# Kernel optimization log

Hardware: AMD Instinct MI355X
Metric: run time of the kernel (lower is better)

The kernel has to match this reference:

```python
import math
import jax, jax.numpy as jnp
import numpy as np

B, T, C, NB = 2, 2048, 512, 4
EPS = 1.1920929e-7  # torch.finfo(float32).eps, used by F.rms_norm default


def rms_norm(x):
    return x * jax.lax.rsqrt(jnp.mean(x * x, axis=-1, keepdims=True) + EPS)


def rope(x):
    # standard rotary embedding over the last dim; x: (..., T, C)
    t_len, c = x.shape[-2], x.shape[-1]
    half = c // 2
    inv_freq = 1.0 / (10000.0 ** (jnp.arange(half, dtype=jnp.float32) / half))
    ang = jnp.arange(t_len, dtype=jnp.float32)[:, None] * inv_freq[None, :]  # (T, half)
    cos, sin = jnp.cos(ang), jnp.sin(ang)
    x1, x2 = x[..., :half], x[..., half:]
    return jnp.concatenate([x1 * cos - x2 * sin, x2 * cos + x1 * sin], axis=-1)


def setup_inputs() -> dict:
    key = jax.random.key(0)
    ks = jax.random.split(key, 8)
    sc = 1.0 / math.sqrt(C)
    return {
        "a": jax.random.normal(ks[0], (B, T, C), jnp.float32),
        "x": jax.random.normal(ks[1], (B, T, C), jnp.float32),
        "Wq": jax.random.normal(ks[2], (C, NB * C), jnp.float32) * sc,
        "Wk": jax.random.normal(ks[3], (C, C), jnp.float32) * sc,
        "Wv": jax.random.normal(ks[4], (C, NB * C), jnp.float32) * sc,
        "Wo": jax.random.normal(ks[5], (C, C), jnp.float32) * sc,
        "v_sink_residual": jax.random.normal(ks[6], (1, 1, 1, C), jnp.float32) * 0.02,
        "v_sink_basis": jax.random.normal(ks[7], (1, NB, 1, C), jnp.float32) * 0.02,
    }


def reference(a, x, Wq, Wk, Wv, Wo, v_sink_residual, v_sink_basis):
    # projections
    q = (a @ Wq).reshape(B, T, NB, C).transpose(0, 2, 1, 3)  # (B,NB,T,C)
    q = rms_norm(q)
    v = (a @ Wv).reshape(B, T, NB, C).transpose(0, 2, 1, 3)  # (B,NB,T,C)
    k = x @ Wk  # (B,T,C), single branch
    q, k = rope(q), rope(k)

    att = jnp.einsum('bntc,bsc->bnts', q, k) / math.sqrt(C)  # (B,NB,T,T)
    causal = jnp.tril(jnp.ones((T, T), dtype=bool))
    att = jnp.where(causal, att, -jnp.inf)

    # branch-axis softmax; fully-masked (non-causal) columns are all -inf -> nan -> 0
    m = jax.lax.stop_gradient(jnp.max(att, axis=1, keepdims=True))
    e = jnp.exp(att - m)
    soft_probs = jnp.nan_to_num(e / jnp.sum(e, axis=1, keepdims=True))

    # hard argmax routing with straight-through estimator
    max_val = jnp.max(soft_probs, axis=1, keepdims=True)
    hard_mask = (soft_probs == max_val).astype(soft_probs.dtype)
    route_mask = jax.lax.stop_gradient(hard_mask - soft_probs) + soft_probs  # (B,NB,T,T)

    # softplus gating on per-position max score
    scores_max = jnp.max(att, axis=1)          # (B,T,T)
    s = jax.nn.softplus(scores_max)            # softplus(-inf) = 0 on masked
    S = jnp.sum(s, axis=-1, keepdims=True)
    scale = jnp.minimum(1.0 / (S + 1e-6), 1.0)
    w = s * scale                              # (B,T,T)
    residual = 1.0 - jnp.sum(w, axis=-1, keepdims=True)  # (B,T,1)

    combined_weights = w[:, None] * route_mask           # (B,NB,T,T)
    y_context = jnp.einsum('bnts,bnsc->bntc', combined_weights, v)
    branch_activity = jnp.max(route_mask, axis=-1, keepdims=True)  # (B,NB,T,1)
    y_basis = branch_activity * v_sink_basis               # (B,NB,T,C)
    y_branches = jnp.sum(y_context + y_basis, axis=1)      # (B,T,C)
    y_res = residual * v_sink_residual[:, 0]               # (B,T,1)*(1,1,C) -> (B,T,C)
    y = y_branches + y_res
    return y @ Wo
```

## Files before the change

### kernel.cpp

```cpp
#include <hip/hip_runtime.h>
#include <math.h>

#define B_    2
#define T_    2048
#define C_    512
#define NB_   4
#define HALF_ 256
#define BT_   (B_*T_)
#define EPS_  1.1920929e-07f
#define RSC_  0.044194173824159216f

using f32x4 = __attribute__((ext_vector_type(4))) float;
using s16x8 = __attribute__((ext_vector_type(8))) short;
using u16x8 = __attribute__((ext_vector_type(8))) unsigned short;

__device__ __forceinline__ unsigned short f2bf(float f) {
    unsigned x = __float_as_uint(f);
    unsigned r = (x + 0x7fffu + ((x >> 16) & 1u)) >> 16;
    return (unsigned short)r;
}
__device__ __forceinline__ float bf2f(unsigned short h) {
    return __uint_as_float(((unsigned)h) << 16);
}

__device__ __forceinline__ void gl16(const void* g, void* l) {
    __builtin_amdgcn_global_load_lds(
        (const __attribute__((address_space(1))) unsigned int*)g,
        (__attribute__((address_space(3))) unsigned int*)l, 16, 0, 0);
}

template<int N> __device__ __forceinline__ void wait_vm() {
    if constexpr (N == 0)      asm volatile("s_waitcnt vmcnt(0)" ::: "memory");
    else if constexpr (N == 4) asm volatile("s_waitcnt vmcnt(4)" ::: "memory");
    else                       asm volatile("s_waitcnt vmcnt(8)" ::: "memory");
}
__device__ __forceinline__ void wait_lgkm0() {
    asm volatile("s_waitcnt lgkmcnt(0)" ::: "memory");
}
__device__ __forceinline__ void bar() { __builtin_amdgcn_s_barrier(); }
__device__ __forceinline__ void sbar0() { __builtin_amdgcn_sched_barrier(0); }

__global__ __launch_bounds__(256) void rope_table_k(float* __restrict__ cosT,
                                                    float* __restrict__ sinT) {
    int t = blockIdx.x;
    int i = threadIdx.x;
    float ex   = (float)i / (float)HALF_;
    float invf = 1.0f / powf(10000.0f, ex);
    float ang  = (float)t * invf;
    float sv, cv;
    sincosf(ang, &sv, &cv);
    cosT[t*HALF_ + i] = cv;
    sinT[t*HALF_ + i] = sv;
}

__global__ __launch_bounds__(256) void cast2_hilo_k(const float* __restrict__ a,
                                                    const float* __restrict__ x,
                                                    unsigned short* __restrict__ ahi,
                                                    unsigned short* __restrict__ alo,
                                                    unsigned short* __restrict__ xhi,
                                                    unsigned short* __restrict__ xlo) {
    int i = blockIdx.x * 256 + threadIdx.x;
    const float* src; unsigned short *hi, *lo;
    if (i < 524288) { src = a; hi = ahi; lo = alo; }
    else { i -= 524288; src = x; hi = xhi; lo = xlo; }
    float4 v = ((const float4*)src)[i];
    ushort4 h, l;
    h.x = f2bf(v.x); l.x = f2bf(v.x - bf2f(h.x));
    h.y = f2bf(v.y); l.y = f2bf(v.y - bf2f(h.y));
    h.z = f2bf(v.z); l.z = f2bf(v.z - bf2f(h.z));
    h.w = f2bf(v.w); l.w = f2bf(v.w - bf2f(h.w));
    ((ushort4*)hi)[i] = h;
    ((ushort4*)lo)[i] = l;
}

__global__ __launch_bounds__(256) void tcast_k(const float* __restrict__ W,
                                               unsigned short* __restrict__ Whi,
                                               unsigned short* __restrict__ Wlo,
                                               int K, int N, int wantLo) {
    __shared__ float tile[64][65];
    int nbt = N >> 6;
    int nb = blockIdx.x % nbt, kb = blockIdx.x / nbt;
    int tid = threadIdx.x;
    int ty = tid >> 6, tx = tid & 63;
    for (int i = ty; i < 64; i += 4)
        tile[i][tx] = W[(size_t)(kb*64 + i) * N + nb*64 + tx];
    __syncthreads();
    for (int j = ty; j < 64; j += 4) {
        float v = tile[tx][j];
        unsigned short h = f2bf(v);
        size_t o = (size_t)(nb*64 + j) * K + kb*64 + tx;
        Whi[o] = h;
        if (wantLo) Wlo[o] = f2bf(v - bf2f(h));
    }
}

template<int SPLIT>
__global__ __launch_bounds__(256, SPLIT ? 2 : 4) void mm_k(
    const unsigned short* __restrict__ Ahi, const unsigned short* __restrict__ Alo,
    const unsigned short* __restrict__ Bhi, const unsigned short* __restrict__ Blo,
    float* __restrict__ C, int M, int N, int K)
{
    constexpr int BUFS = SPLIT ? 16384 : 8192;
    __shared__ __align__(16) short smem[2 * BUFS];

    int tid = threadIdx.x;
    int w = tid >> 6, l = tid & 63;
    int wm = w >> 1, wn = w & 1;
    int llo = l & 15, lhi = l >> 4;
    int rl8 = l >> 3, sl8 = l & 7;
    int nwg = gridDim.x;
    int bid = blockIdx.x;
    int sb = (bid & 7) * (nwg >> 3) + (bid >> 3);
    int nbt = N >> 7;
    int bx = sb % nbt, by = sb / nbt;
    int m0 = by << 7, n0 = bx << 7;

    const unsigned short* hs[4];
    const unsigned short* ls[4];
    int dst_[4];
    #pragma unroll
    for (int c = 0; c < 4; c++) {
        int r = (w << 5) + (c << 3) + rl8;
        int sp = sl8 ^ (r & 7);
        size_t off = (sp < 4) ? ((size_t)(m0 + r) * K + (sp << 3))
                              : ((size_t)(n0 + r) * K + ((sp - 4) << 3));
        hs[c] = (sp < 4 ? Ahi : Bhi) + off;
        if constexpr (SPLIT) ls[c] = (sp < 4 ? Alo : Blo) + off;
        dst_[c] = (w << 11) + (c << 9);
    }
    auto STAGE = [&](int cur, int k0) {
        short* base = smem + cur * BUFS;
        #pragma unroll
        for (int c = 0; c < 4; c++) {
            gl16(hs[c] + k0, base + dst_[c]);
            if constexpr (SPLIT) gl16(ls[c] + k0, base + 8192 + dst_[c]);
        }
    };

    f32x4 acc[4][4];
    #pragma unroll
    for (int mi = 0; mi < 4; mi++)
        #pragma unroll
        for (int ni = 0; ni < 4; ni++) acc[mi][ni] = (f32x4){0.f,0.f,0.f,0.f};

    const int NK = K >> 5;
    STAGE(0, 0);
    int cur = 0;
    for (int k = 0; k < NK; k++) {
        if (k + 1 < NK) { STAGE(cur ^ 1, (k + 1) << 5); wait_vm<SPLIT ? 8 : 4>(); }
        else wait_vm<0>();
        bar(); sbar0();
        short* Mh = smem + cur * BUFS;
        short* Ml = Mh + 8192;
        s16x8 bh[4], bl[4];
        #pragma unroll
        for (int ni = 0; ni < 4; ni++) {
            int br = (wn << 6) + (ni << 4) + llo;
            int bo = (br << 6) + (((lhi | 4) ^ (br & 7)) << 3);
            bh[ni] = *(const s16x8*)&Mh[bo];
            if constexpr (SPLIT) bl[ni] = *(const s16x8*)&Ml[bo];
        }
        #pragma unroll
        for (int mi = 0; mi < 4; mi++) {
            int ar = (wm << 6) + (mi << 4) + llo;
            int ao = (ar << 6) + ((lhi ^ (ar & 7)) << 3);
            s16x8 ah = *(const s16x8*)&Mh[ao];
            s16x8 al;
            if constexpr (SPLIT) al = *(const s16x8*)&Ml[ao];
            #pragma unroll
            for (int ni = 0; ni < 4; ni++) {
                acc[mi][ni] = __builtin_amdgcn_mfma_f32_16x16x32_bf16(ah, bh[ni], acc[mi][ni], 0, 0, 0);
                if constexpr (SPLIT) {
                    acc[mi][ni] = __builtin_amdgcn_mfma_f32_16x16x32_bf16(ah, bl[ni], acc[mi][ni], 0, 0, 0);
                    acc[mi][ni] = __builtin_amdgcn_mfma_f32_16x16x32_bf16(al, bh[ni], acc[mi][ni], 0, 0, 0);
                }
            }
        }
        wait_lgkm0(); sbar0(); bar();
        cur ^= 1;
    }
    #pragma unroll
    for (int mi = 0; mi < 4; mi++) {
        int row0 = m0 + (wm << 6) + (mi << 4) + (lhi << 2);
        #pragma unroll
        for (int ni = 0; ni < 4; ni++) {
            int col = n0 + (wn << 6) + (ni << 4) + llo;
            f32x4 v = acc[mi][ni];
            #pragma unroll
            for (int r = 0; r < 4; r++)
                C[(size_t)(row0 + r) * N + col] = v[r];
        }
    }
}

__global__ __launch_bounds__(256, 4) void mm_v_k(
    const unsigned short* __restrict__ Ahi,
    const unsigned short* __restrict__ Bhi,
    unsigned short* __restrict__ Vt, int M, int N, int K)
{
    __shared__ __align__(16) short smem[2 * 8192];
    int tid = threadIdx.x;
    int w = tid >> 6, l = tid & 63;
    int wm = w >> 1, wn = w & 1;
    int llo = l & 15, lhi = l >> 4;
    int rl8 = l >> 3, sl8 = l & 7;
    int nwg = gridDim.x;
    int bid = blockIdx.x;
    int sb = (bid & 7) * (nwg >> 3) + (bid >> 3);
    int nbt = N >> 7;
    int bx = sb % nbt, by = sb / nbt;
    int m0 = by << 7, n0 = bx << 7;

    const unsigned short* hs[4];
    int dst_[4];
    #pragma unroll
    for (int c = 0; c < 4; c++) {
        int r = (w << 5) + (c << 3) + rl8;
        int sp = sl8 ^ (r & 7);
        size_t off = (sp < 4) ? ((size_t)(m0 + r) * K + (sp << 3))
                              : ((size_t)(n0 + r) * K + ((sp - 4) << 3));
        hs[c] = (sp < 4 ? Ahi : Bhi) + off;
        dst_[c] = (w << 11) + (c << 9);
    }
    auto STAGE = [&](int cur, int k0) {
        short* base = smem + cur * 8192;
        #pragma unroll
        for (int c = 0; c < 4; c++) gl16(hs[c] + k0, base + dst_[c]);
    };

    f32x4 acc[4][4];
    #pragma unroll
    for (int mi = 0; mi < 4; mi++)
        #pragma unroll
        for (int ni = 0; ni < 4; ni++) acc[mi][ni] = (f32x4){0.f,0.f,0.f,0.f};

    const int NK = K >> 5;
    STAGE(0, 0);
    int cur = 0;
    for (int k = 0; k < NK; k++) {
        if (k + 1 < NK) { STAGE(cur ^ 1, (k + 1) << 5); wait_vm<4>(); }
        else wait_vm<0>();
        bar(); sbar0();
        short* Mh = smem + cur * 8192;
        s16x8 bh[4];
        #pragma unroll
        for (int ni = 0; ni < 4; ni++) {
            int br = (wn << 6) + (ni << 4) + llo;
            bh[ni] = *(const s16x8*)&Mh[(br << 6) + (((lhi | 4) ^ (br & 7)) << 3)];
        }
        #pragma unroll
        for (int mi = 0; mi < 4; mi++) {
            int ar = (wm << 6) + (mi << 4) + llo;
            s16x8 ah = *(const s16x8*)&Mh[(ar << 6) + ((lhi ^ (ar & 7)) << 3)];
            #pragma unroll
            for (int ni = 0; ni < 4; ni++)
                acc[mi][ni] = __builtin_amdgcn_mfma_f32_16x16x32_bf16(ah, bh[ni], acc[mi][ni], 0, 0, 0);
        }
        wait_lgkm0(); sbar0(); bar();
        cur ^= 1;
    }
    #pragma unroll
    for (int mi = 0; mi < 4; mi++) {
        int row0 = m0 + (wm << 6) + (mi << 4) + (lhi << 2);
        int b = row0 >> 11, t = row0 & (T_ - 1);
        #pragma unroll
        for (int ni = 0; ni < 4; ni++) {
            int col = n0 + (wn << 6) + (ni << 4) + llo;
            f32x4 v = acc[mi][ni];
            ushort4 o;
            o.x = f2bf(v[0]); o.y = f2bf(v[1]); o.z = f2bf(v[2]); o.w = f2bf(v[3]);
            *(ushort4*)(Vt + ((size_t)(b*(NB_*C_) + col)) * T_ + t) = o;
        }
    }
}

__global__ __launch_bounds__(256) void q_post3_k(const float* __restrict__ Qf,
                                                 const float* __restrict__ cosT,
                                                 const float* __restrict__ sinT,
                                                 unsigned short* __restrict__ Qhi,
                                                 unsigned short* __restrict__ Qlo) {
    int bt = blockIdx.x;
    int t  = bt & (T_ - 1);
    int w = threadIdx.x >> 6, l = threadIdx.x & 63;
    const float* row = Qf + (size_t)bt * (NB_*C_) + (w << 9);
    int i0 = l << 2;
    float4 x1 = *(const float4*)(row + i0);
    float4 x2 = *(const float4*)(row + i0 + HALF_);
    float s = x1.x*x1.x + x1.y*x1.y + x1.z*x1.z + x1.w*x1.w
            + x2.x*x2.x + x2.y*x2.y + x2.z*x2.z + x2.w*x2.w;
    #pragma unroll
    for (int mask = 1; mask <= 32; mask <<= 1) s += __shfl_xor(s, mask, 64);
    float r = rsqrtf(s * (1.0f / (float)C_) + EPS_);
    float4 cv = *(const float4*)(cosT + t*HALF_ + i0);
    float4 sv = *(const float4*)(sinT + t*HALF_ + i0);
    float v1[4], v2[4];
    v1[0] = x1.x*r*cv.x - x2.x*r*sv.x;  v2[0] = x2.x*r*cv.x + x1.x*r*sv.x;
    v1[1] = x1.y*r*cv.y - x2.y*r*sv.y;  v2[1] = x2.y*r*cv.y + x1.y*r*sv.y;
    v1[2] = x1.z*r*cv.z - x2.z*r*sv.z;  v2[2] = x2.z*r*cv.z + x1.z*r*sv.z;
    v1[3] = x1.w*r*cv.w - x2.w*r*sv.w;  v2[3] = x2.w*r*cv.w + x1.w*r*sv.w;
    size_t o = (size_t)bt * (NB_*C_) + (w << 9) + i0;
    ushort4 h1, h2, l1, l2;
    h1.x = f2bf(v1[0]); l1.x = f2bf(v1[0] - bf2f(h1.x));
    h1.y = f2bf(v1[1]); l1.y = f2bf(v1[1] - bf2f(h1.y));
    h1.z = f2bf(v1[2]); l1.z = f2bf(v1[2] - bf2f(h1.z));
    h1.w = f2bf(v1[3]); l1.w = f2bf(v1[3] - bf2f(h1.w));
    h2.x = f2bf(v2[0]); l2.x = f2bf(v2[0] - bf2f(h2.x));
    h2.y = f2bf(v2[1]); l2.y = f2bf(v2[1] - bf2f(h2.y));
    h2.z = f2bf(v2[2]); l2.z = f2bf(v2[2] - bf2f(h2.z));
    h2.w = f2bf(v2[3]); l2.w = f2bf(v2[3] - bf2f(h2.w));
    *(ushort4*)(Qhi + o)          = h1;
    *(ushort4*)(Qhi + o + HALF_)  = h2;
    *(ushort4*)(Qlo + o)          = l1;
    *(ushort4*)(Qlo + o + HALF_)  = l2;
}

__global__ __launch_bounds__(256) void k_post3_k(const float* __restrict__ Kf,
                                                 const float* __restrict__ cosT,
                                                 const float* __restrict__ sinT,
                                                 unsigned short* __restrict__ Khi,
                                                 unsigned short* __restrict__ Klo) {
    int sub = threadIdx.x >> 7, l = threadIdx.x & 127;
    int bt = blockIdx.x * 2 + sub;
    int t  = bt & (T_ - 1);
    const float* row = Kf + (size_t)bt * C_;
    int i0 = l << 1;
    float2 x1 = *(const float2*)(row + i0);
    float2 x2 = *(const float2*)(row + i0 + HALF_);
    float2 cv = *(const float2*)(cosT + t*HALF_ + i0);
    float2 sv = *(const float2*)(sinT + t*HALF_ + i0);
    float v1x = x1.x*cv.x - x2.x*sv.x, v2x = x2.x*cv.x + x1.x*sv.x;
    float v1y = x1.y*cv.y - x2.y*sv.y, v2y = x2.y*cv.y + x1.y*sv.y;
    size_t o = (size_t)bt * C_ + i0;
    ushort2 h1, h2, l1, l2;
    h1.x = f2bf(v1x); l1.x = f2bf(v1x - bf2f(h1.x));
    h1.y = f2bf(v1y); l1.y = f2bf(v1y - bf2f(h1.y));
    h2.x = f2bf(v2x); l2.x = f2bf(v2x - bf2f(h2.x));
    h2.y = f2bf(v2y); l2.y = f2bf(v2y - bf2f(h2.y));
    *(ushort2*)(Khi + o)         = h1;
    *(ushort2*)(Khi + o + HALF_) = h2;
    *(ushort2*)(Klo + o)         = l1;
    *(ushort2*)(Klo + o + HALF_) = l2;
}

__global__ __launch_bounds__(256, 2) void qk_routing_k(
    const unsigned short* __restrict__ Qhi, const unsigned short* __restrict__ Qlo,
    const unsigned short* __restrict__ Khi, const unsigned short* __restrict__ Klo,
    unsigned short* __restrict__ P, float* __restrict__ partS, unsigned* __restrict__ partA)
{
    __shared__ __align__(16) short smem[32768];

    int tid = threadIdx.x;
    int w = tid >> 6, l = tid & 63;
    int wm = w >> 1, wn = w & 1;
    int llo = l & 15, lhi = l >> 4;
    int rl8 = l >> 3, sl8 = l & 7;

    int bid = blockIdx.x;
    int j = (bid & 7) * 136 + (bid >> 3);
    int b = (j >= 544) ? 1 : 0;
    int j2 = j - 544 * b;
    int q = (int)((sqrtf(1.0f + 2.0f*(float)j2) - 1.0f) * 0.5f);
    if (2*(q+1)*(q+2) <= j2) q++;
    if (2*q*(q+1) > j2) q--;
    int r0 = j2 - 2*q*(q+1);
    int tloc = r0 / (q+1);
    int st = r0 - tloc*(q+1);
    int tt = (q << 2) + tloc;
    int t0 = tt << 5, s0 = st << 7;

    const unsigned short* hsrc[4];
    const unsigned short* lsrc[4];
    int dst_[4];
    #pragma unroll
    for (int c = 0; c < 4; c++) {
        int r = (w << 5) + (c << 3) + rl8;
        int sp = sl8 ^ (r & 7);
        size_t off = (sp < 4)
            ? ((size_t)(b*T_ + t0 + (r >> 2)) * (NB_*C_) + ((r & 3) << 9) + (sp << 3))
            : ((size_t)(b*T_ + s0 + r) * C_ + ((sp - 4) << 3));
        hsrc[c] = (sp < 4 ? Qhi : Khi) + off;
        lsrc[c] = (sp < 4 ? Qlo : Klo) + off;
        dst_[c] = (w << 11) + (c << 9);
    }
    auto STAGE = [&](int cur, int k0) {
        short* base = smem + (cur << 14);
        #pragma unroll
        for (int c = 0; c < 4; c++) {
            gl16(hsrc[c] + k0, base + dst_[c]);
            gl16(lsrc[c] + k0, base + 8192 + dst_[c]);
        }
    };

    f32x4 acc[4][4];
    #pragma unroll
    for (int mi = 0; mi < 4; mi++)
        #pragma unroll
        for (int ni = 0; ni < 4; ni++) acc[mi][ni] = (f32x4){0.f,0.f,0.f,0.f};

    STAGE(0, 0);
    int cur = 0;
    for (int k = 0; k < 16; k++) {
        if (k + 1 < 16) { STAGE(cur ^ 1, (k + 1) << 5); wait_vm<8>(); }
        else wait_vm<0>();
        bar(); sbar0();
        short* Mh = smem + (cur << 14);
        short* Ml = Mh + 8192;
        s16x8 bh[4], bl[4];
        #pragma unroll
        for (int ni = 0; ni < 4; ni++) {
            int br = (wn << 6) + (ni << 4) + llo;
            int bo = (br << 6) + (((lhi | 4) ^ (br & 7)) << 3);
            bh[ni] = *(const s16x8*)&Mh[bo];
            bl[ni] = *(const s16x8*)&Ml[bo];
        }
        #pragma unroll
        for (int mi = 0; mi < 4; mi++) {
            int ar = (wm << 6) + (mi << 4) + llo;
            int ao = (ar << 6) + ((lhi ^ (ar & 7)) << 3);
            s16x8 ah = *(const s16x8*)&Mh[ao];
            s16x8 al = *(const s16x8*)&Ml[ao];
            #pragma unroll
            for (int ni = 0; ni < 4; ni++) {
                acc[mi][ni] = __builtin_amdgcn_mfma_f32_16x16x32_bf16(ah, bh[ni], acc[mi][ni], 0, 0, 0);
                acc[mi][ni] = __builtin_amdgcn_mfma_f32_16x16x32_bf16(ah, bl[ni], acc[mi][ni], 0, 0, 0);
                acc[mi][ni] = __builtin_amdgcn_mfma_f32_16x16x32_bf16(al, bh[ni], acc[mi][ni], 0, 0, 0);
            }
        }
        wait_lgkm0(); sbar0(); bar();
        cur ^= 1;
    }
    __syncthreads();

    short* Pl = smem;
    #pragma unroll
    for (int mi = 0; mi < 4; mi++) {
        int tl = (wm << 4) + (mi << 2) + lhi;
        int tg = t0 + tl;
        float wsum = 0.f; unsigned ab = 0u;
        #pragma unroll
        for (int ni = 0; ni < 4; ni++) {
            int sl = (wn << 6) + (ni << 4) + llo;
            int sg = s0 + sl;
            f32x4 v = acc[mi][ni];
            float wu = 0.f; unsigned bits = 0u;
            if (sg <= tg) {
                float a0 = v[0]*RSC_, a1 = v[1]*RSC_, a2 = v[2]*RSC_, a3 = v[3]*RSC_;
                float m = fmaxf(fmaxf(a0, a1), fmaxf(a2, a3));
                bits = (a0 == m ? 1u : 0u) | (a1 == m ? 2u : 0u)
                     | (a2 == m ? 4u : 0u) | (a3 == m ? 8u : 0u);
                wu = fmaxf(m, 0.f) + log1pf(expf(-fabsf(m)));
                wsum += wu; ab |= bits;
            }
            unsigned short wub = f2bf(wu);
            Pl[(0*32 + tl)*136 + sl] = (bits & 1u) ? (short)wub : (short)0;
            Pl[(1*32 + tl)*136 + sl] = (bits & 2u) ? (short)wub : (short)0;
            Pl[(2*32 + tl)*136 + sl] = (bits & 4u) ? (short)wub : (short)0;
            Pl[(3*32 + tl)*136 + sl] = (bits & 8u) ? (short)wub : (short)0;
        }
        #pragma unroll
        for (int mask = 1; mask <= 8; mask <<= 1) wsum += __shfl_xor(wsum, mask, 64);
        int ai = (int)ab;
        #pragma unroll
        for (int mask = 1; mask <= 8; mask <<= 1) ai |= __shfl_xor(ai, mask, 64);
        if (llo == 0) {
            size_t pidx = ((((size_t)(b*64 + tt) * 16 + st) * 2 + wn) * 32) + tl;
            partS[pidx] = wsum;
            partA[pidx] = (unsigned)ai;
        }
    }
    __syncthreads();
    for (int i = tid; i < 2048; i += 256) {
        int row = i >> 4, g8 = i & 15;
        int n = row >> 5, tl = row & 31;
        u16x8 v = *(const u16x8*)&Pl[row*136 + (g8 << 3)];
        *(u16x8*)(P + ((size_t)((b*4 + n)*T_ + t0 + tl)) * T_ + s0 + (g8 << 3)) = v;
    }
}

__global__ __launch_bounds__(256, 2) void pv_k(
    const unsigned short* __restrict__ P, const unsigned short* __restrict__ Vt,
    unsigned short* __restrict__ py)
{
    __shared__ __align__(16) short smem[32768];
    int tid = threadIdx.x;
    int w = tid >> 6, l = tid & 63;
    int wm = w >> 1, wn = w & 1;
    int llo = l & 15, lhi = l >> 4;
    int rl = l >> 3, gs8 = l & 7;
    int rb = w << 5;
    int bid = blockIdx.x;
    int ph = bid & 3, cc = (bid >> 2) & 3, tt = 15 - ((bid >> 4) & 15), b = bid >> 8;
    int t0 = tt << 7, c0 = cc << 7;
    int b4 = b * 4;
    size_t bV = (size_t)b * (NB_*C_);

    size_t pa_[4], pb_[4];
    int dsb_[4];
    #pragma unroll
    for (int i8 = 0; i8 < 4; i8++) {
        int r = rb + (i8 << 3) + rl;
        int sg = (gs8 ^ (r & 7)) << 3;
        pa_[i8] = (size_t)(t0 + r) * T_ + sg;
        pb_[i8] = (size_t)(c0 + r) * T_ + sg;
        dsb_[i8] = (rb + (i8 << 3)) << 6;
    }
    auto STAGE = [&](int cur, int n, int k0) {
        short* base = smem + (cur << 14);
        size_t na = (size_t)(b4 + n) * T_ * T_;
        size_t nb = (bV + (size_t)(n << 9)) * T_;
        #pragma unroll
        for (int i8 = 0; i8 < 4; i8++) {
            gl16(P  + na + pa_[i8] + k0, base + dsb_[i8]);
            gl16(Vt + nb + pb_[i8] + k0, base + 8192 + dsb_[i8]);
        }
    };

    f32x4 acc[4][4];
    #pragma unroll
    for (int mi = 0; mi < 4; mi++)
        #pragma unroll
        for (int ni = 0; ni < 4; ni++) acc[mi][ni] = (f32x4){0.f,0.f,0.f,0.f};

    int first_sb = ph << 7;
    int num_sb = (first_sb <= t0 + 127) ? (((t0 + 127 - first_sb) >> 9) + 1) : 0;
    int nsteps = num_sb << 3;

    if (nsteps > 0) {
        int n_p = 0, sb_p = first_sb, h_p = 0;
        auto ADV = [&]() {
            h_p ^= 1;
            if (!h_p) { sb_p += 512; if (sb_p > t0 + 127) { sb_p = first_sb; n_p++; } }
        };
        STAGE(0, n_p, sb_p + (h_p << 6)); ADV();
        int cur = 0;
        for (int s = 0; s < nsteps; s++) {
            if (s + 1 < nsteps) { STAGE(cur ^ 1, n_p, sb_p + (h_p << 6)); ADV(); wait_vm<8>(); }
            else wait_vm<0>();
            bar(); sbar0();
            short* Ah = smem + (cur << 14);
            short* Bh = Ah + 8192;
            #pragma unroll
            for (int ks = 0; ks < 2; ks++) {
                s16x8 bh[4];
                #pragma unroll
                for (int ni = 0; ni < 4; ni++) {
                    int br = (wn << 6) + (ni << 4) + llo;
                    bh[ni] = *(const s16x8*)&Bh[br*64 + ((((ks << 2) + lhi) ^ (br & 7)) << 3)];
                }
                #pragma unroll
                for (int mi = 0; mi < 4; mi++) {
                    int ar = (wm << 6) + (mi << 4) + llo;
                    s16x8 ah = *(const s16x8*)&Ah[ar*64 + ((((ks << 2) + lhi) ^ (ar & 7)) << 3)];
                    #pragma unroll
                    for (int ni = 0; ni < 4; ni++)
                        acc[mi][ni] = __builtin_amdgcn_mfma_f32_16x16x32_bf16(ah, bh[ni], acc[mi][ni], 0, 0, 0);
                }
            }
            wait_lgkm0(); sbar0(); bar();
            cur ^= 1;
        }
    }
    unsigned short* out = py + (size_t)ph * (BT_*(size_t)C_);
    #pragma unroll
    for (int mi = 0; mi < 4; mi++) {
        int row0 = t0 + (wm << 6) + (mi << 4) + (lhi << 2);
        #pragma unroll
        for (int ni = 0; ni < 4; ni++) {
            int col = c0 + (wn << 6) + (ni << 4) + llo;
            f32x4 v = acc[mi][ni];
            #pragma unroll
            for (int r = 0; r < 4; r++)
                out[(size_t)(b*T_ + row0 + r) * C_ + col] = f2bf(v[r]);
        }
    }
}

__global__ __launch_bounds__(256) void combine3_k(
    const unsigned short* __restrict__ py, const float* __restrict__ partS,
    const unsigned* __restrict__ partA,
    const float* __restrict__ basis, const float* __restrict__ resid_sink,
    unsigned short* __restrict__ ybf)
{
    int bt = blockIdx.x;
    int t = bt & (T_ - 1);
    int b = bt >> 11;
    int i = threadIdx.x;
    int tt32 = t >> 5, tl = t & 31;
    int stmax = tt32 >> 2;
    float S = 0.f; unsigned act = 0u;
    for (int st = 0; st <= stmax; st++) {
        #pragma unroll
        for (int wn = 0; wn < 2; wn++) {
            size_t idx = ((((size_t)(b*64 + tt32) * 16 + st) * 2 + wn) * 32) + tl;
            S += partS[idx];
            act |= partA[idx];
        }
    }
    float y0 = 0.f, y1 = 0.f;
    #pragma unroll
    for (int ph = 0; ph < 4; ph++) {
        y0 += bf2f(py[(size_t)ph * (BT_*(size_t)C_) + (size_t)bt * C_ + i]);
        y1 += bf2f(py[(size_t)ph * (BT_*(size_t)C_) + (size_t)bt * C_ + i + 256]);
    }
    float scale = fminf(1.0f / (S + 1e-6f), 1.0f);
    float residual = 1.0f - scale * S;
    if (t < T_ - 1) act = 0xFu;
    float o0 = scale * y0, o1 = scale * y1;
    #pragma unroll
    for (int n = 0; n < 4; n++) if ((act >> n) & 1u) {
        o0 += basis[n*C_ + i];
        o1 += basis[n*C_ + i + 256];
    }
    o0 += residual * resid_sink[i];
    o1 += residual * resid_sink[i + 256];
    ybf[(size_t)bt * C_ + i]       = f2bf(o0);
    ybf[(size_t)bt * C_ + i + 256] = f2bf(o1);
}

extern "C" void kernel_launch(void* const* d_in, const int* in_sizes, int n_in,
                              void* d_out, int out_size, void* d_ws, size_t ws_size,
                              hipStream_t stream) {
    const float* a    = (const float*)d_in[0];
    const float* x    = (const float*)d_in[1];
    const float* Wq   = (const float*)d_in[2];
    const float* Wk   = (const float*)d_in[3];
    const float* Wv   = (const float*)d_in[4];
    const float* Wo   = (const float*)d_in[5];
    const float* vres = (const float*)d_in[6];
    const float* vbas = (const float*)d_in[7];

    float* ws = (float*)d_ws;
    float* cosT = ws;
    float* sinT = cosT + 524288;
    float* Qf   = sinT + 524288;
    float* Kf   = Qf + 8388608;
    unsigned short* ahi  = (unsigned short*)(Kf + 2097152);
    unsigned short* alo  = ahi  + 2097152;
    unsigned short* xhi  = alo  + 2097152;
    unsigned short* xlo  = xhi  + 2097152;
    unsigned short* Wqth = xlo  + 2097152;
    unsigned short* Wqtl = Wqth + 1048576;
    unsigned short* Wkth = Wqtl + 1048576;
    unsigned short* Wktl = Wkth + 262144;
    unsigned short* Wvth = Wktl + 262144;
    unsigned short* Woth = Wvth + 1048576;
    unsigned short* Qhi  = Woth + 262144;
    unsigned short* Qlo  = Qhi  + 8388608;
    unsigned short* Khi  = Qlo  + 8388608;
    unsigned short* Klo  = Khi  + 2097152;
    unsigned short* Vt   = Klo  + 2097152;
    unsigned short* P    = Vt   + 8388608;

    unsigned short* py = (unsigned short*)Qf;
    float* partS = Kf;
    unsigned* partA = (unsigned*)(Kf + 131072);
    unsigned short* ybf = (unsigned short*)(Kf + 262144);

    rope_table_k<<<T_, 256, 0, stream>>>(cosT, sinT);
    cast2_hilo_k<<<4096, 256, 0, stream>>>(a, x, ahi, alo, xhi, xlo);
    tcast_k<<<256, 256, 0, stream>>>(Wq, Wqth, Wqtl, 512, 2048, 1);
    tcast_k<<<64,  256, 0, stream>>>(Wk, Wkth, Wktl, 512, 512,  1);
    tcast_k<<<256, 256, 0, stream>>>(Wv, Wvth, nullptr, 512, 2048, 0);
    tcast_k<<<64,  256, 0, stream>>>(Wo, Woth, nullptr, 512, 512,  0);

    mm_k<1><<<512, 256, 0, stream>>>(ahi, alo, Wqth, Wqtl, Qf, BT_, 2048, 512);
    mm_k<1><<<128, 256, 0, stream>>>(xhi, xlo, Wkth, Wktl, Kf, BT_, 512, 512);
    mm_v_k<<<512, 256, 0, stream>>>(ahi, Wvth, Vt, BT_, 2048, 512);

    q_post3_k<<<BT_, 256, 0, stream>>>(Qf, cosT, sinT, Qhi, Qlo);
    k_post3_k<<<BT_/2, 256, 0, stream>>>(Kf, cosT, sinT, Khi, Klo);

    qk_routing_k<<<1088, 256, 0, stream>>>(Qhi, Qlo, Khi, Klo, P, partS, partA);
    pv_k<<<512, 256, 0, stream>>>(P, Vt, py);
    combine3_k<<<BT_, 256, 0, stream>>>(py, partS, partA, vbas, vres, ybf);

    mm_k<0><<<128, 256, 0, stream>>>(ybf, nullptr, Woth, nullptr, (float*)d_out, BT_, 512, 512);
}
```

Before: 238.9 us.

## Split K-loop into two phases interleaving hi/lo prefetch with MFMA and setprio

Restructures the score-GEMM main loop into two half-phases: the hi-part prefetch is issued before the first MFMA half and the lo-part prefetch between halves, with A-fragment LDS reads split accordingly. MFMA blocks are wrapped in s_setprio(1) and extra barriers are added so the phases of different waves line up. The intent is to overlap global-to-LDS copies and LDS reads with matrix math rather than bunching all loads at the top of each iteration. It adds more barriers per iteration and splits the vmcnt waits, which could cost more than the overlap gains.

```diff
diff --git a/kernel.cpp b/kernel.cpp
--- a/kernel.cpp
+++ b/kernel.cpp
@@ -382,14 +382,6 @@
         lsrc[c] = (sp < 4 ? Qlo : Klo) + off;
         dst_[c] = (w << 11) + (c << 9);
     }
-    auto STAGE = [&](int cur, int k0) {
-        short* base = smem + (cur << 14);
-        #pragma unroll
-        for (int c = 0; c < 4; c++) {
-            gl16(hsrc[c] + k0, base + dst_[c]);
-            gl16(lsrc[c] + k0, base + 8192 + dst_[c]);
-        }
-    };
 
     f32x4 acc[4][4];
     #pragma unroll
@@ -397,14 +389,26 @@
         #pragma unroll
         for (int ni = 0; ni < 4; ni++) acc[mi][ni] = (f32x4){0.f,0.f,0.f,0.f};
 
-    STAGE(0, 0);
+    {
+        short* base = smem;
+        #pragma unroll
+        for (int c = 0; c < 4; c++) gl16(hsrc[c], base + dst_[c]);
+        #pragma unroll
+        for (int c = 0; c < 4; c++) gl16(lsrc[c], base + 8192 + dst_[c]);
+    }
     int cur = 0;
     for (int k = 0; k < 16; k++) {
-        if (k + 1 < 16) { STAGE(cur ^ 1, (k + 1) << 5); wait_vm<8>(); }
-        else wait_vm<0>();
-        bar(); sbar0();
         short* Mh = smem + (cur << 14);
         short* Ml = Mh + 8192;
+        short* Nb = smem + ((cur ^ 1) << 14);
+        int k1 = (k + 1) << 5;
+
+        if (k < 15) {
+            #pragma unroll
+            for (int c = 0; c < 4; c++) gl16(hsrc[c] + k1, Nb + dst_[c]);
+            wait_vm<4>();
+        } else wait_vm<0>();
+        bar(); sbar0();
         s16x8 bh[4], bl[4];
         #pragma unroll
         for (int ni = 0; ni < 4; ni++) {
@@ -413,20 +417,70 @@
             bh[ni] = *(const s16x8*)&Mh[bo];
             bl[ni] = *(const s16x8*)&Ml[bo];
         }
-        #pragma unroll
-        for (int mi = 0; mi < 4; mi++) {
-            int ar = (wm << 6) + (mi << 4) + llo;
+        s16x8 ah0, al0, ah1, al1;
+        {
+            int ar = (wm << 6) + llo;
             int ao = (ar << 6) + ((lhi ^ (ar & 7)) << 3);
-            s16x8 ah = *(const s16x8*)&Mh[ao];
-            s16x8 al = *(const s16x8*)&Ml[ao];
+            ah0 = *(const s16x8*)&Mh[ao];
+            al0 = *(const s16x8*)&Ml[ao];
+        }
+        {
+            int ar = (wm << 6) + 16 + llo;
+            int ao = (ar << 6) + ((lhi ^ (ar & 7)) << 3);
+            ah1 = *(const s16x8*)&Mh[ao];
+            al1 = *(const s16x8*)&Ml[ao];
+        }
+        wait_lgkm0(); sbar0();
+        __builtin_amdgcn_s_setprio(1);
+        #pragma unroll
+        for (int ni = 0; ni < 4; ni++) {
+            acc[0][ni] = __builtin_amdgcn_mfma_f32_16x16x32_bf16(ah0, bh[ni], acc[0][ni], 0, 0, 0);
+            acc[0][ni] = __builtin_amdgcn_mfma_f32_16x16x32_bf16(ah0, bl[ni], acc[0][ni], 0, 0, 0);
+            acc[0][ni] = __builtin_amdgcn_mfma_f32_16x16x32_bf16(al0, bh[ni], acc[0][ni], 0, 0, 0);
+        }
+        #pragma unroll
+        for (int ni = 0; ni < 4; ni++) {
+            acc[1][ni] = __builtin_amdgcn_mfma_f32_16x16x32_bf16(ah1, bh[ni], acc[1][ni], 0, 0, 0);
+            acc[1][ni] = __builtin_amdgcn_mfma_f32_16x16x32_bf16(ah1, bl[ni], acc[1][ni], 0, 0, 0);
+            acc[1][ni] = __builtin_amdgcn_mfma_f32_16x16x32_bf16(al1, bh[ni], acc[1][ni], 0, 0, 0);
+        }
+        __builtin_amdgcn_s_setprio(0);
+        bar();
+
+        if (k < 15) {
             #pragma unroll
-            for (int ni = 0; ni < 4; ni++) {
-                acc[mi][ni] = __builtin_amdgcn_mfma_f32_16x16x32_bf16(ah, bh[ni], acc[mi][ni], 0, 0, 0);
-                acc[mi][ni] = __builtin_amdgcn_mfma_f32_16x16x32_bf16(ah, bl[ni], acc[mi][ni], 0, 0, 0);
-                acc[mi][ni] = __builtin_amdgcn_mfma_f32_16x16x32_bf16(al, bh[ni], acc[mi][ni], 0, 0, 0);
-            }
-        }
-        wait_lgkm0(); sbar0(); bar();
+            for (int c = 0; c < 4; c++) gl16(lsrc[c] + k1, Nb + 8192 + dst_[c]);
+        }
+        s16x8 ah2, al2, ah3, al3;
+        {
+            int ar = (wm << 6) + 32 + llo;
+            int ao = (ar << 6) + ((lhi ^ (ar & 7)) << 3);
+            ah2 = *(const s16x8*)&Mh[ao];
+            al2 = *(const s16x8*)&Ml[ao];
+        }
+        {
+            int ar = (wm << 6) + 48 + llo;
+            int ao = (ar << 6) + ((lhi ^ (ar & 7)) << 3);
+            ah3 = *(const s16x8*)&Mh[ao];
+            al3 = *(const s16x8*)&Ml[ao];
+        }
+        bar();
+        wait_lgkm0(); sbar0();
+        __builtin_amdgcn_s_setprio(1);
+        #pragma unroll
+        for (int ni = 0; ni < 4; ni++) {
+            acc[2][ni] = __builtin_amdgcn_mfma_f32_16x16x32_bf16(ah2, bh[ni], acc[2][ni], 0, 0, 0);
+            acc[2][ni] = __builtin_amdgcn_mfma_f32_16x16x32_bf16(ah2, bl[ni], acc[2][ni], 0, 0, 0);
+            acc[2][ni] = __builtin_amdgcn_mfma_f32_16x16x32_bf16(al2, bh[ni], acc[2][ni], 0, 0, 0);
+        }
+        #pragma unroll
+        for (int ni = 0; ni < 4; ni++) {
+            acc[3][ni] = __builtin_amdgcn_mfma_f32_16x16x32_bf16(ah3, bh[ni], acc[3][ni], 0, 0, 0);
+            acc[3][ni] = __builtin_amdgcn_mfma_f32_16x16x32_bf16(ah3, bl[ni], acc[3][ni], 0, 0, 0);
+            acc[3][ni] = __builtin_amdgcn_mfma_f32_16x16x32_bf16(al3, bh[ni], acc[3][ni], 0, 0, 0);
+        }
+        __builtin_amdgcn_s_setprio(0);
+        bar();
         cur ^= 1;
     }
     __syncthreads();
```

Result: no change. 240.5 us (+0.7%).
